# Optimization experiments

Measured on AMD Instinct MI355X. Metric: run time of the kernel, lower is better.

## Reference

```python
import jax, jax.numpy as jnp
import numpy as np

B, T, V = 512, 200, 2048
E, H, I, A = 20, 100, 64, 32  # embedding, hidden, intermediate, actions


def setup_inputs() -> dict:
    key = jax.random.key(0)
    ks = jax.random.split(key, 12)
    batch = jax.random.uniform(ks[0], (B, T, V), dtype=jnp.float32)
    lengths = jax.random.randint(ks[1], (B,), 1, T + 1)
    s = 0.05
    W_emb = jax.random.normal(ks[2], (E, V), dtype=jnp.float32) * s
    b_emb = jnp.zeros((E,), jnp.float32)
    W_ih = jax.random.normal(ks[3], (4 * H, E), dtype=jnp.float32) * s
    W_hh = jax.random.normal(ks[4], (4 * H, H), dtype=jnp.float32) * s
    b_ih = jnp.zeros((4 * H,), jnp.float32)
    # torch init sets forget-gate bias (second quarter) to 1.0 in bias_hh
    b_hh = jnp.zeros((4 * H,), jnp.float32).at[H:2 * H].set(1.0)
    W1 = jax.random.normal(ks[5], (I, H), dtype=jnp.float32) * s
    b1 = jnp.zeros((I,), jnp.float32)
    W2 = jax.random.normal(ks[6], (A, I), dtype=jnp.float32) * s
    b2 = jnp.zeros((A,), jnp.float32)
    h0 = jnp.zeros((B, H), jnp.float32)
    c0 = jnp.zeros((B, H), jnp.float32)
    return {"batch": batch, "lengths": lengths, "W_emb": W_emb, "b_emb": b_emb,
            "W_ih": W_ih, "W_hh": W_hh, "b_ih": b_ih, "b_hh": b_hh,
            "W1": W1, "b1": b1, "W2": W2, "b2": b2, "h0": h0, "c0": c0}


def reference(batch, lengths, W_emb, b_emb, W_ih, W_hh, b_ih, b_hh,
              W1, b1, W2, b2, h0, c0):
    # Embedding via Linear: [B,T,V] @ [V,E] -> [B,T,E]
    emb = jnp.einsum('btv,ev->bte', batch, W_emb) + b_emb
    # Precompute input contribution to all gates: [B,T,4H]
    xg = jnp.einsum('bte,ge->btg', emb, W_ih) + b_ih + b_hh

    def step(carry, xg_t):
        h, c = carry
        gates = xg_t + h @ W_hh.T  # [B,4H]
        i, f, g, o = jnp.split(gates, 4, axis=-1)  # torch gate order i,f,g,o
        c = jax.nn.sigmoid(f) * c + jax.nn.sigmoid(i) * jnp.tanh(g)
        h = jax.nn.sigmoid(o) * jnp.tanh(c)
        return (h, c), h

    _, ys = jax.lax.scan(step, (h0, c0), jnp.swapaxes(xg, 0, 1))  # ys: [T,B,H]
    nb = batch.shape[0]
    h_final = ys[lengths - 1, jnp.arange(nb)]  # [B,H] output at last valid step
    inter = jax.nn.relu(h_final @ W1.T + b1)
    actions = inter @ W2.T + b2
    return actions
```

## Files before the change

kernel.cpp:

```cpp
#include <hip/hip_runtime.h>

#define BB 512
#define TT 200
#define VV 2048
#define EE 20
#define HH 100
#define G4 400
#define II 64
#define AA 32

typedef float vf2 __attribute__((ext_vector_type(2)));

#define WS_WT_OFF  1024
#define WS_EMB_OFF (1024 + VV * EE)

__global__ __launch_bounds__(512) void k0_prep(
    const int* __restrict__ lengths, const float* __restrict__ W_emb,
    int* __restrict__ off, float* __restrict__ Wt)
{
    if (blockIdx.x == 0) {
        __shared__ int s[BB];
        int tid = threadIdx.x;
        s[tid] = lengths[tid];
        __syncthreads();
        for (int d = 1; d < BB; d <<= 1) {
            int v = (tid >= d) ? s[tid - d] : 0;
            __syncthreads();
            if (tid >= d) s[tid] += v;
            __syncthreads();
        }
        off[tid + 1] = s[tid];
        if (tid == 0) off[0] = 0;
    } else {
        int idx = (blockIdx.x - 1) * 512 + threadIdx.x;
        if (idx < VV * EE) {
            int k = idx / EE, e = idx - k * EE;
            Wt[idx] = W_emb[(size_t)e * VV + k];
        }
    }
}

#define R1   128
#define KC   64
#define TSTR 68

__global__ __launch_bounds__(128) void k1_embed(
    const float* __restrict__ batch, const int* __restrict__ off,
    const float* __restrict__ Wt, const float* __restrict__ b_emb,
    float* __restrict__ emb)
{
    __shared__ float tile[R1 * TSTR];
    __shared__ float wch[(KC / 2) * EE * 2];
    __shared__ int   roff[R1];

    const int tid  = threadIdx.x;
    const int Nv   = off[BB];
    const int row0 = blockIdx.x * R1;
    if (row0 >= Nv) return;

    const int row    = row0 + tid;
    const bool active = row < Nv;

    int b = 0;
    {
        const int r = active ? row : 0;
        int lo = 0, hi = BB;
        while (lo + 1 < hi) {
            int mid = (lo + hi) >> 1;
            if (off[mid] <= r) lo = mid; else hi = mid;
        }
        b = lo;
    }
    const int t = (active ? row : 0) - off[b];
    roff[tid] = b * TT + t;
    __syncthreads();

    const float* srcp[16];
#pragma unroll
    for (int i = 0; i < 16; ++i) {
        int r = (tid >> 4) + 8 * i;
        srcp[i] = batch + (size_t)roff[r] * VV + (tid & 15) * 4;
    }

    vf2 acc[EE];
#pragma unroll
    for (int e = 0; e < EE; ++e) { acc[e].x = 0.f; acc[e].y = 0.f; }

#pragma unroll 1
    for (int c0 = 0; c0 < VV; c0 += KC) {
        __syncthreads();
#pragma unroll
        for (int i = 0; i < 16; ++i) {
            int r = (tid >> 4) + 8 * i;
            float4 v = *reinterpret_cast<const float4*>(srcp[i] + c0);
            *reinterpret_cast<float4*>(&tile[r * TSTR + (tid & 15) * 4]) = v;
        }
#pragma unroll
        for (int i = 0; i < 10; ++i) {
            int l = tid + i * 128;
            int k = l / EE, e = l - k * EE;
            wch[(k >> 1) * (2 * EE) + e * 2 + (k & 1)] = Wt[(size_t)c0 * EE + l];
        }
        __syncthreads();
#pragma unroll
        for (int p = 0; p < 16; ++p) {
            float4 xv = *reinterpret_cast<const float4*>(&tile[tid * TSTR + p * 4]);
            vf2 xlo, xhi;
            xlo.x = xv.x; xlo.y = xv.y;
            xhi.x = xv.z; xhi.y = xv.w;
            const float* wlo = &wch[(2 * p) * (2 * EE)];
            const float* whi = &wch[(2 * p + 1) * (2 * EE)];
#pragma unroll
            for (int e2 = 0; e2 < EE / 2; ++e2) {
                float4 wv = *reinterpret_cast<const float4*>(wlo + e2 * 4);
                vf2 w0, w1;
                w0.x = wv.x; w0.y = wv.y;
                w1.x = wv.z; w1.y = wv.w;
                acc[2 * e2]     = __builtin_elementwise_fma(w0, xlo, acc[2 * e2]);
                acc[2 * e2 + 1] = __builtin_elementwise_fma(w1, xlo, acc[2 * e2 + 1]);
            }
#pragma unroll
            for (int e2 = 0; e2 < EE / 2; ++e2) {
                float4 wv = *reinterpret_cast<const float4*>(whi + e2 * 4);
                vf2 w0, w1;
                w0.x = wv.x; w0.y = wv.y;
                w1.x = wv.z; w1.y = wv.w;
                acc[2 * e2]     = __builtin_elementwise_fma(w0, xhi, acc[2 * e2]);
                acc[2 * e2 + 1] = __builtin_elementwise_fma(w1, xhi, acc[2 * e2 + 1]);
            }
        }
    }

    if (active) {
        float o[EE];
#pragma unroll
        for (int e = 0; e < EE; ++e) o[e] = acc[e].x + acc[e].y + b_emb[e];
        float* dst = emb + (size_t)(b * TT + t) * EE;
#pragma unroll
        for (int e = 0; e < EE; e += 4)
            *reinterpret_cast<float4*>(dst + e) = make_float4(o[e], o[e+1], o[e+2], o[e+3]);
    }
}

__device__ __forceinline__ float fast_sig(float x) { return 1.f / (1.f + __expf(-x)); }
__device__ __forceinline__ float fast_tanh(float x) {
    x = fminf(fmaxf(x, -15.f), 15.f);
    float e = __expf(2.f * x);
    return (e - 1.f) / (e + 1.f);
}
__device__ __forceinline__ float dpp_xor1_add(float v) {
    int p = __builtin_amdgcn_update_dpp(0, __builtin_bit_cast(int, v), 0xB1, 0xF, 0xF, true);
    return v + __builtin_bit_cast(float, p);
}
__device__ __forceinline__ float dpp_xor2_add(float v) {
    int p = __builtin_amdgcn_update_dpp(0, __builtin_bit_cast(int, v), 0x4E, 0xF, 0xF, true);
    return v + __builtin_bit_cast(float, p);
}
#define QSTR 36

__global__ __launch_bounds__(448) void k2_lstm(
    const float* __restrict__ emb, const int* __restrict__ lengths,
    const float* __restrict__ W_ih, const float* __restrict__ W_hh,
    const float* __restrict__ b_ih, const float* __restrict__ b_hh,
    const float* __restrict__ W1, const float* __restrict__ b1,
    const float* __restrict__ W2, const float* __restrict__ b2,
    const float* __restrict__ h0, const float* __restrict__ c0,
    float* __restrict__ out)
{
    __shared__ float xhbuf[2][2][160];
    __shared__ float hfin[2][HH];
    __shared__ float inter[2][II];

    const int tid = threadIdx.x;
    const int b0  = blockIdx.x * 2;
    const int len0 = lengths[b0];
    const int len1 = lengths[b0 + 1];
    const int tmax = (len0 > len1) ? len0 : len1;

    const int j = tid >> 2, q = tid & 3;

    for (int i = tid; i < 2 * 2 * 160; i += 448) (&xhbuf[0][0][0])[i] = 0.f;

    vf2 w2[4][16];
    float biasv[4];
    float c_reg = 0.f;
    int lenq = 0;
    if (tid < G4) {
        const int rr[4] = { j, HH + j, 2 * HH + j, 3 * HH + j };
#pragma unroll
        for (int g = 0; g < 4; ++g) {
            const int r = rr[g];
#pragma unroll
            for (int mp = 0; mp < 16; ++mp) {
                int k = q * 32 + mp * 2;
                float2 v;
                if (k + 1 < EE)          v = *reinterpret_cast<const float2*>(&W_ih[r * EE + k]);
                else if (k + 1 < EE + HH) v = *reinterpret_cast<const float2*>(&W_hh[r * HH + k - EE]);
                else                     v = make_float2(0.f, 0.f);
                w2[g][mp].x = v.x; w2[g][mp].y = v.y;
            }
            biasv[g] = b_ih[r] + b_hh[r];
        }
        if (q < 2) c_reg = c0[(size_t)(b0 + q) * HH + j];
        lenq = (q == 0) ? len0 : len1;
    }
    __syncthreads();

    float xreg = 0.f;
    if (tid < G4) {
        if (q < 2) {
            int i = EE + j;
            xhbuf[0][q][(i >> 5) * QSTR + (i & 31)] = h0[(size_t)(b0 + q) * HH + j];
        }
    } else if (tid < G4 + 2 * EE) {
        const int wdx = tid - G4, bw = wdx / EE, e = wdx - bw * EE;
        const float* ep = emb + (size_t)(b0 + bw) * TT * EE;
        xhbuf[0][bw][e] = ep[e];
        xreg = ep[EE + e];
    }
    __syncthreads();

#pragma unroll 1
    for (int t = 0; t < tmax; ++t) {
        const int cur = t & 1, nxt = cur ^ 1;
        if (tid < G4) {
            vf2 a[4][2];
#pragma unroll
            for (int g = 0; g < 4; ++g) { a[g][0].x=0.f; a[g][0].y=0.f; a[g][1].x=0.f; a[g][1].y=0.f; }
            const float* xc = &xhbuf[cur][0][0];
#pragma unroll
            for (int m8 = 0; m8 < 8; ++m8) {
                float4 x0 = *reinterpret_cast<const float4*>(xc + q * QSTR + m8 * 4);
                float4 x1 = *reinterpret_cast<const float4*>(xc + 160 + q * QSTR + m8 * 4);
                vf2 xl0, xh0, xl1, xh1;
                xl0.x = x0.x; xl0.y = x0.y;  xh0.x = x0.z; xh0.y = x0.w;
                xl1.x = x1.x; xl1.y = x1.y;  xh1.x = x1.z; xh1.y = x1.w;
#pragma unroll
                for (int g = 0; g < 4; ++g) {
                    a[g][0] = __builtin_elementwise_fma(w2[g][2*m8],   xl0, a[g][0]);
                    a[g][0] = __builtin_elementwise_fma(w2[g][2*m8+1], xh0, a[g][0]);
                    a[g][1] = __builtin_elementwise_fma(w2[g][2*m8],   xl1, a[g][1]);
                    a[g][1] = __builtin_elementwise_fma(w2[g][2*m8+1], xh1, a[g][1]);
                }
            }
            float s_[4][2];
#pragma unroll
            for (int g = 0; g < 4; ++g) {
#pragma unroll
                for (int bb = 0; bb < 2; ++bb) {
                    float v = a[g][bb].x + a[g][bb].y;
                    v = dpp_xor1_add(v);
                    v = dpp_xor2_add(v);
                    s_[g][bb] = v;
                }
            }
            if (q < 2) {
                float gi = s_[0][q] + biasv[0];
                float gf = s_[1][q] + biasv[1];
                float gg = s_[2][q] + biasv[2];
                float go = s_[3][q] + biasv[3];
                c_reg = fast_sig(gf) * c_reg + fast_sig(gi) * fast_tanh(gg);
                float hv = fast_sig(go) * fast_tanh(c_reg);
                int i = EE + j;
                xhbuf[nxt][q][(i >> 5) * QSTR + (i & 31)] = hv;
                if (t == lenq - 1) hfin[q][j] = hv;
            }
        } else if (tid < G4 + 2 * EE) {
            const int wdx = tid - G4, bw = wdx / EE, e = wdx - bw * EE;
            xhbuf[nxt][bw][e] = xreg;
            xreg = (t + 2 < TT)
                 ? emb[((size_t)(b0 + bw) * TT + (t + 2)) * EE + e] : 0.f;
        }
        __syncthreads();
    }

    if (tid < 2 * II) {
        int bb = tid >> 6, i = tid & 63;
        float a = b1[i];
        const float* w1r = W1 + i * HH;
#pragma unroll
        for (int k = 0; k < HH; k += 4) {
            a += w1r[k] * hfin[bb][k] + w1r[k+1] * hfin[bb][k+1]
               + w1r[k+2] * hfin[bb][k+2] + w1r[k+3] * hfin[bb][k+3];
        }
        inter[bb][i] = fmaxf(a, 0.f);
    }
    __syncthreads();
    if (tid < 2 * AA) {
        int bb = tid >> 5, ai = tid & 31;
        float a = b2[ai];
        const float* w2r = W2 + ai * II;
#pragma unroll
        for (int k = 0; k < II; ++k) a += w2r[k] * inter[bb][k];
        out[(size_t)(b0 + bb) * AA + ai] = a;
    }
}

extern "C" void kernel_launch(void* const* d_in, const int* in_sizes, int n_in,
                              void* d_out, int out_size, void* d_ws, size_t ws_size,
                              hipStream_t stream) {
    const float* batch  = (const float*)d_in[0];
    const int*   lengths= (const int*)  d_in[1];
    const float* W_emb  = (const float*)d_in[2];
    const float* b_emb  = (const float*)d_in[3];
    const float* W_ih   = (const float*)d_in[4];
    const float* W_hh   = (const float*)d_in[5];
    const float* b_ih   = (const float*)d_in[6];
    const float* b_hh   = (const float*)d_in[7];
    const float* W1     = (const float*)d_in[8];
    const float* b1     = (const float*)d_in[9];
    const float* W2     = (const float*)d_in[10];
    const float* b2     = (const float*)d_in[11];
    const float* h0     = (const float*)d_in[12];
    const float* c0     = (const float*)d_in[13];
    float* out = (float*)d_out;

    int*   off = (int*)d_ws;
    float* Wt  = (float*)d_ws + WS_WT_OFF;
    float* emb = (float*)d_ws + WS_EMB_OFF;

    k0_prep<<<1 + (VV * EE + 511) / 512, 512, 0, stream>>>(lengths, W_emb, off, Wt);
    k1_embed<<<(BB * TT + R1 - 1) / R1, R1, 0, stream>>>(batch, off, Wt, b_emb, emb);
    k2_lstm<<<BB / 2, 448, 0, stream>>>(emb, lengths, W_ih, W_hh, b_ih, b_hh,
                                        W1, b1, W2, b2, h0, c0, out);
}
```

Before: 445.3 us.

## Compute embedding projection with fp16 MFMA using pre-swizzled weight fragments

Replaces the FP32 shared-memory tiled embedding GEMM with a per-wavefront MFMA 16x16x32 fp16 kernel. Batch rows are loaded straight from global memory, converted to fp16 in registers, and multiplied against W_emb fragments that the prep kernel pre-arranges in the MFMA operand layout. The aim is to cut the FP32 ALU and LDS cost of the projection so the step is limited by streaming the batch. In exchange, inputs and weights are rounded to fp16, which loses precision, and the output columns are padded to 32.

```diff
diff --git a/kernel.cpp b/kernel.cpp
--- a/kernel.cpp
+++ b/kernel.cpp
@@ -9,14 +9,17 @@
 #define II 64
 #define AA 32
 
-typedef float vf2 __attribute__((ext_vector_type(2)));
-
-#define WS_WT_OFF  1024
-#define WS_EMB_OFF (1024 + VV * EE)
+typedef _Float16 half8 __attribute__((ext_vector_type(8)));
+typedef float    f32x4 __attribute__((ext_vector_type(4)));
+typedef float    vf2   __attribute__((ext_vector_type(2)));
+
+#define NCHUNK 64
+#define WS_BF_OFF  1024
+#define WS_EMB_OFF (1024 + 32768)
 
 __global__ __launch_bounds__(512) void k0_prep(
     const int* __restrict__ lengths, const float* __restrict__ W_emb,
-    int* __restrict__ off, float* __restrict__ Wt)
+    int* __restrict__ off, _Float16* __restrict__ Bfrag)
 {
     if (blockIdx.x == 0) {
         __shared__ int s[BB];
@@ -32,113 +35,72 @@
         off[tid + 1] = s[tid];
         if (tid == 0) off[0] = 0;
     } else {
-        int idx = (blockIdx.x - 1) * 512 + threadIdx.x;
-        if (idx < VV * EE) {
-            int k = idx / EE, e = idx - k * EE;
-            Wt[idx] = W_emb[(size_t)e * VV + k];
-        }
-    }
-}
-
-#define R1   128
-#define KC   64
-#define TSTR 68
-
-__global__ __launch_bounds__(128) void k1_embed(
+        int F = (blockIdx.x - 1) * 512 + threadIdx.x;
+        if (F < NCHUNK * 2 * 64 * 8) {
+            int e = F & 7, l = (F >> 3) & 63, n = (F >> 9) & 1, c = F >> 10;
+            int k = c * 32 + (l >> 4) * 8 + e;
+            int col = n * 16 + (l & 15);
+            float v = (col < EE) ? W_emb[(size_t)col * VV + k] : 0.f;
+            Bfrag[F] = (_Float16)v;
+        }
+    }
+}
+
+__global__ __launch_bounds__(256) void k1_embed(
     const float* __restrict__ batch, const int* __restrict__ off,
-    const float* __restrict__ Wt, const float* __restrict__ b_emb,
+    const _Float16* __restrict__ Bfrag, const float* __restrict__ b_emb,
     float* __restrict__ emb)
 {
-    __shared__ float tile[R1 * TSTR];
-    __shared__ float wch[(KC / 2) * EE * 2];
-    __shared__ int   roff[R1];
-
-    const int tid  = threadIdx.x;
-    const int Nv   = off[BB];
-    const int row0 = blockIdx.x * R1;
-    if (row0 >= Nv) return;
-
-    const int row    = row0 + tid;
-    const bool active = row < Nv;
-
-    int b = 0;
-    {
-        const int r = active ? row : 0;
-        int lo = 0, hi = BB;
-        while (lo + 1 < hi) {
-            int mid = (lo + hi) >> 1;
-            if (off[mid] <= r) lo = mid; else hi = mid;
-        }
-        b = lo;
-    }
-    const int t = (active ? row : 0) - off[b];
-    roff[tid] = b * TT + t;
-    __syncthreads();
-
-    const float* srcp[16];
-#pragma unroll
-    for (int i = 0; i < 16; ++i) {
-        int r = (tid >> 4) + 8 * i;
-        srcp[i] = batch + (size_t)roff[r] * VV + (tid & 15) * 4;
-    }
-
-    vf2 acc[EE];
-#pragma unroll
-    for (int e = 0; e < EE; ++e) { acc[e].x = 0.f; acc[e].y = 0.f; }
-
-#pragma unroll 1
-    for (int c0 = 0; c0 < VV; c0 += KC) {
-        __syncthreads();
-#pragma unroll
-        for (int i = 0; i < 16; ++i) {
-            int r = (tid >> 4) + 8 * i;
-            float4 v = *reinterpret_cast<const float4*>(srcp[i] + c0);
-            *reinterpret_cast<float4*>(&tile[r * TSTR + (tid & 15) * 4]) = v;
-        }
-#pragma unroll
-        for (int i = 0; i < 10; ++i) {
-            int l = tid + i * 128;
-            int k = l / EE, e = l - k * EE;
-            wch[(k >> 1) * (2 * EE) + e * 2 + (k & 1)] = Wt[(size_t)c0 * EE + l];
-        }
-        __syncthreads();
-#pragma unroll
-        for (int p = 0; p < 16; ++p) {
-            float4 xv = *reinterpret_cast<const float4*>(&tile[tid * TSTR + p * 4]);
-            vf2 xlo, xhi;
-            xlo.x = xv.x; xlo.y = xv.y;
-            xhi.x = xv.z; xhi.y = xv.w;
-            const float* wlo = &wch[(2 * p) * (2 * EE)];
-            const float* whi = &wch[(2 * p + 1) * (2 * EE)];
-#pragma unroll
-            for (int e2 = 0; e2 < EE / 2; ++e2) {
-                float4 wv = *reinterpret_cast<const float4*>(wlo + e2 * 4);
-                vf2 w0, w1;
-                w0.x = wv.x; w0.y = wv.y;
-                w1.x = wv.z; w1.y = wv.w;
-                acc[2 * e2]     = __builtin_elementwise_fma(w0, xlo, acc[2 * e2]);
-                acc[2 * e2 + 1] = __builtin_elementwise_fma(w1, xlo, acc[2 * e2 + 1]);
-            }
-#pragma unroll
-            for (int e2 = 0; e2 < EE / 2; ++e2) {
-                float4 wv = *reinterpret_cast<const float4*>(whi + e2 * 4);
-                vf2 w0, w1;
-                w0.x = wv.x; w0.y = wv.y;
-                w1.x = wv.z; w1.y = wv.w;
-                acc[2 * e2]     = __builtin_elementwise_fma(w0, xhi, acc[2 * e2]);
-                acc[2 * e2 + 1] = __builtin_elementwise_fma(w1, xhi, acc[2 * e2 + 1]);
-            }
-        }
-    }
-
-    if (active) {
-        float o[EE];
-#pragma unroll
-        for (int e = 0; e < EE; ++e) o[e] = acc[e].x + acc[e].y + b_emb[e];
-        float* dst = emb + (size_t)(b * TT + t) * EE;
-#pragma unroll
-        for (int e = 0; e < EE; e += 4)
-            *reinterpret_cast<float4*>(dst + e) = make_float4(o[e], o[e+1], o[e+2], o[e+3]);
+    const int Nv = off[BB];
+    if (blockIdx.x * 64 >= Nv) return;
+
+    const int lane  = threadIdx.x & 63;
+    const int wid   = threadIdx.x >> 6;
+    const int rbase = blockIdx.x * 64 + wid * 16;
+
+    int lrow = rbase + (lane & 15);
+    int lr = (lrow < Nv) ? lrow : (Nv - 1);
+    int lo = 0, hi = BB;
+    while (lo + 1 < hi) {
+        int mid = (lo + hi) >> 1;
+        if (off[mid] <= lr) lo = mid; else hi = mid;
+    }
+    const int lroff = lo * TT + (lr - off[lo]);
+
+    const float* __restrict__ aptr = batch + (size_t)lroff * VV + ((lane >> 4) * 8);
+    const half8* __restrict__ bptr = reinterpret_cast<const half8*>(Bfrag) + lane;
+
+    f32x4 acc0 = {0.f, 0.f, 0.f, 0.f};
+    f32x4 acc1 = {0.f, 0.f, 0.f, 0.f};
+
+#pragma unroll 4
+    for (int c = 0; c < NCHUNK; ++c) {
+        float4 a0 = *reinterpret_cast<const float4*>(aptr + c * 32);
+        float4 a1 = *reinterpret_cast<const float4*>(aptr + c * 32 + 4);
+        half8 b0 = bptr[(c * 2 + 0) * 64];
+        half8 b1 = bptr[(c * 2 + 1) * 64];
+        half8 av;
+        av[0] = (_Float16)a0.x; av[1] = (_Float16)a0.y;
+        av[2] = (_Float16)a0.z; av[3] = (_Float16)a0.w;
+        av[4] = (_Float16)a1.x; av[5] = (_Float16)a1.y;
+        av[6] = (_Float16)a1.z; av[7] = (_Float16)a1.w;
+        acc0 = __builtin_amdgcn_mfma_f32_16x16x32_f16(av, b0, acc0, 0, 0, 0);
+        acc1 = __builtin_amdgcn_mfma_f32_16x16x32_f16(av, b1, acc1, 0, 0, 0);
+    }
+
+    const int col0 = lane & 15;
+    const float bias0 = b_emb[col0];
+    const float bias1 = (col0 < 4) ? b_emb[16 + col0] : 0.f;
+#pragma unroll
+    for (int r = 0; r < 4; ++r) {
+        int s = (lane >> 4) * 4 + r;
+        int srow = rbase + s;
+        int sroff = __shfl(lroff, s, 64);
+        if (srow < Nv) {
+            emb[(size_t)sroff * EE + col0] = acc0[r] + bias0;
+            if (col0 < 4)
+                emb[(size_t)sroff * EE + 16 + col0] = acc1[r] + bias1;
+        }
     }
 }
 
@@ -194,9 +156,9 @@
             for (int mp = 0; mp < 16; ++mp) {
                 int k = q * 32 + mp * 2;
                 float2 v;
-                if (k + 1 < EE)          v = *reinterpret_cast<const float2*>(&W_ih[r * EE + k]);
+                if (k + 1 < EE)           v = *reinterpret_cast<const float2*>(&W_ih[r * EE + k]);
                 else if (k + 1 < EE + HH) v = *reinterpret_cast<const float2*>(&W_hh[r * HH + k - EE]);
-                else                     v = make_float2(0.f, 0.f);
+                else                      v = make_float2(0.f, 0.f);
                 w2[g][mp].x = v.x; w2[g][mp].y = v.y;
             }
             biasv[g] = b_ih[r] + b_hh[r];
@@ -261,8 +223,8 @@
                 float go = s_[3][q] + biasv[3];
                 c_reg = fast_sig(gf) * c_reg + fast_sig(gi) * fast_tanh(gg);
                 float hv = fast_sig(go) * fast_tanh(c_reg);
-                int i = EE + j;
-                xhbuf[nxt][q][(i >> 5) * QSTR + (i & 31)] = hv;
+                int ii = EE + j;
+                xhbuf[nxt][q][(ii >> 5) * QSTR + (ii & 31)] = hv;
                 if (t == lenq - 1) hfin[q][j] = hv;
             }
         } else if (tid < G4 + 2 * EE) {
@@ -315,12 +277,12 @@
     const float* c0     = (const float*)d_in[13];
     float* out = (float*)d_out;
 
-    int*   off = (int*)d_ws;
-    float* Wt  = (float*)d_ws + WS_WT_OFF;
-    float* emb = (float*)d_ws + WS_EMB_OFF;
-
-    k0_prep<<<1 + (VV * EE + 511) / 512, 512, 0, stream>>>(lengths, W_emb, off, Wt);
-    k1_embed<<<(BB * TT + R1 - 1) / R1, R1, 0, stream>>>(batch, off, Wt, b_emb, emb);
+    int*       off   = (int*)d_ws;
+    _Float16*  Bfrag = (_Float16*)((float*)d_ws + WS_BF_OFF);
+    float*     emb   = (float*)d_ws + WS_EMB_OFF;
+
+    k0_prep<<<1 + (NCHUNK * 2 * 64 * 8 + 511) / 512, 512, 0, stream>>>(lengths, W_emb, off, Bfrag);
+    k1_embed<<<(BB * TT + 63) / 64, 256, 0, stream>>>(batch, off, Bfrag, b_emb, emb);
     k2_lstm<<<BB / 2, 448, 0, stream>>>(emb, lengths, W_ih, W_hh, b_ih, b_hh,
                                         W1, b1, W2, b2, h0, c0, out);
 }
```

Measured after the change: 402.2 us. 1.11x faster.
